# Kernel tuning notes

Measured on AMD Instinct MI355X. Metric: run time of the kernel, lower is better.

Reference implementation:

```python
import jax, jax.numpy as jnp
import numpy as np

N_NODES = 50000
N_EDGES = 800000
D_NODE = 64
D_EDGE = 64


def setup_inputs() -> dict:
    key = jax.random.key(0)
    ks = jax.random.split(key, 6)
    node_scalars = jax.random.normal(ks[0], (N_NODES, D_NODE), dtype=jnp.float32)
    edge_feats = jax.random.normal(ks[1], (N_EDGES, D_EDGE), dtype=jnp.float32)
    src_idxs = jax.random.randint(ks[2], (N_EDGES,), 0, N_NODES, dtype=jnp.int32)
    dst_idxs = jax.random.randint(ks[3], (N_EDGES,), 0, N_NODES, dtype=jnp.int32)
    in_dim = 2 * D_NODE + D_EDGE  # 192
    # He-ish init for the MLP weights
    W1 = jax.random.normal(ks[4], (in_dim, D_EDGE), dtype=jnp.float32) / np.sqrt(in_dim)
    b1 = jnp.zeros((D_EDGE,), dtype=jnp.float32)
    W2 = jax.random.normal(ks[5], (D_EDGE, D_EDGE), dtype=jnp.float32) / np.sqrt(D_EDGE)
    b2 = jnp.zeros((D_EDGE,), dtype=jnp.float32)
    ln_gamma = jnp.ones((D_EDGE,), dtype=jnp.float32)
    ln_beta = jnp.zeros((D_EDGE,), dtype=jnp.float32)
    return {
        "node_scalars": node_scalars,
        "edge_feats": edge_feats,
        "src_idxs": src_idxs,
        "dst_idxs": dst_idxs,
        "W1": W1,
        "b1": b1,
        "W2": W2,
        "b2": b2,
        "ln_gamma": ln_gamma,
        "ln_beta": ln_beta,
    }


def _layer_norm(x, gamma, beta, eps=1e-5):
    mu = jnp.mean(x, axis=-1, keepdims=True)
    var = jnp.mean(jnp.square(x - mu), axis=-1, keepdims=True)
    return (x - mu) * jax.lax.rsqrt(var + eps) * gamma + beta


def reference(node_scalars, edge_feats, src_idxs, dst_idxs, W1, b1, W2, b2, ln_gamma, ln_beta):
    # gather endpoint node features per edge and concat with edge feats -> [E, 2*Dn + De]
    mlp_in = jnp.concatenate(
        [node_scalars[src_idxs], node_scalars[dst_idxs], edge_feats], axis=-1
    )
    h = jax.nn.silu(mlp_in @ W1 + b1)
    h = jax.nn.silu(h @ W2 + b2)
    return _layer_norm(edge_feats + h, ln_gamma, ln_beta)
```

## Files before the change

### kernel.cpp

```cpp
#include <hip/hip_runtime.h>

#define NE 800000
#define D  64
#define K1 192

typedef __bf16 bf16x8 __attribute__((ext_vector_type(8)));
typedef float  f32x4  __attribute__((ext_vector_type(4)));

__global__ void prep_weights(const float* __restrict__ W1,
                             const float* __restrict__ W2,
                             __bf16* __restrict__ ws) {
  int i = blockIdx.x * 256 + threadIdx.x;
  if (i < K1 * D) {
    int k = i >> 6, n = i & 63;
    ws[n * K1 + k] = (__bf16)W1[i];
  } else {
    int j = i - K1 * D;
    int k = j >> 6, n = j & 63;
    ws[K1 * D + n * D + k] = (__bf16)W2[j];
  }
}

template <bool USE_WS>
__global__ __launch_bounds__(256, 3)
void edge_kernel(const float* __restrict__ nodes, const float* __restrict__ ef,
                 const int* __restrict__ srci, const int* __restrict__ dsti,
                 const float* __restrict__ W1, const float* __restrict__ b1,
                 const float* __restrict__ W2, const float* __restrict__ b2,
                 const float* __restrict__ gmm, const float* __restrict__ bta,
                 const __bf16* __restrict__ wsw, float* __restrict__ out) {
  __shared__ __align__(16) __bf16 w1t[64 * 200];
  __shared__ __align__(16) __bf16 w2t[64 * 72];
  __shared__ __align__(16) __bf16 hbuf[4][16 * 72];
  __shared__ float sb1[64], sb2[64], sg[64], sbt[64];

  const int tid = threadIdx.x;

  if (USE_WS) {
    const uint2* s1 = (const uint2*)wsw;
    for (int c = tid; c < 3072; c += 256) {
      int n = c / 48, kc = c - n * 48;
      *(uint2*)&w1t[n * 200 + kc * 4] = s1[c];
    }
    const uint2* s2 = (const uint2*)(wsw + K1 * D);
    for (int c = tid; c < 1024; c += 256) {
      int n = c >> 4, kc = c & 15;
      *(uint2*)&w2t[n * 72 + kc * 4] = s2[c];
    }
  } else {
    for (int i = tid; i < K1 * D; i += 256) {
      int k = i >> 6, n = i & 63;
      w1t[n * 200 + k] = (__bf16)W1[i];
    }
    for (int i = tid; i < D * D; i += 256) {
      int k = i >> 6, n = i & 63;
      w2t[n * 72 + k] = (__bf16)W2[i];
    }
  }
  if (tid < 64)       sb1[tid]       = b1[tid];
  else if (tid < 128) sb2[tid - 64]  = b2[tid - 64];
  else if (tid < 192) sg[tid - 128]  = gmm[tid - 128];
  else                sbt[tid - 192] = bta[tid - 192];
  __syncthreads();

  const int wave = tid >> 6, lane = tid & 63;
  const int quad = lane >> 4, m16 = lane & 15;
  __bf16* hw = hbuf[wave];

  #pragma unroll 1
  for (int t = 0; t < 4; ++t) {
    const int base = blockIdx.x * 256 + wave * 64 + t * 16;
    const int eRow = base + m16;
    const int s = srci[eRow], d = dsti[eRow];
    const float* r0 = nodes + (size_t)s * D;
    const float* r1 = nodes + (size_t)d * D;
    const float* r2 = ef + (size_t)eRow * D;

    f32x4 acc[4] = {};
    #pragma unroll
    for (int ki = 0; ki < 6; ++ki) {
      const float* p;
      if (ki < 2)      p = r0 + ki * 32 + quad * 8;
      else if (ki < 4) p = r1 + (ki - 2) * 32 + quad * 8;
      else             p = r2 + (ki - 4) * 32 + quad * 8;
      f32x4 lo = *(const f32x4*)p;
      f32x4 hi = *(const f32x4*)(p + 4);
      bf16x8 a;
      a[0] = (__bf16)lo[0]; a[1] = (__bf16)lo[1];
      a[2] = (__bf16)lo[2]; a[3] = (__bf16)lo[3];
      a[4] = (__bf16)hi[0]; a[5] = (__bf16)hi[1];
      a[6] = (__bf16)hi[2]; a[7] = (__bf16)hi[3];
      const int wk = ki * 32 + quad * 8;
      #pragma unroll
      for (int nt = 0; nt < 4; ++nt) {
        bf16x8 bf = *(const bf16x8*)&w1t[(nt * 16 + m16) * 200 + wk];
        acc[nt] = __builtin_amdgcn_mfma_f32_16x16x32_bf16(a, bf, acc[nt], 0, 0, 0);
      }
    }

    #pragma unroll
    for (int nt = 0; nt < 4; ++nt) {
      const int c = nt * 16 + m16;
      const float bb = sb1[c];
      #pragma unroll
      for (int r = 0; r < 4; ++r) {
        float x = acc[nt][r] + bb;
        float sv = x / (1.f + __expf(-x));
        hw[(quad * 4 + r) * 72 + c] = (__bf16)sv;
      }
    }
    __syncthreads();

    f32x4 acc2[4] = {};
    #pragma unroll
    for (int ki = 0; ki < 2; ++ki) {
      bf16x8 a = *(const bf16x8*)&hw[m16 * 72 + ki * 32 + quad * 8];
      #pragma unroll
      for (int nt = 0; nt < 4; ++nt) {
        bf16x8 bf = *(const bf16x8*)&w2t[(nt * 16 + m16) * 72 + ki * 32 + quad * 8];
        acc2[nt] = __builtin_amdgcn_mfma_f32_16x16x32_bf16(a, bf, acc2[nt], 0, 0, 0);
      }
    }

    #pragma unroll
    for (int r = 0; r < 4; ++r) {
      const int row = quad * 4 + r;
      const size_t eo = (size_t)(base + row) * D;
      float x[4];
      float sum = 0.f;
      #pragma unroll
      for (int nt = 0; nt < 4; ++nt) {
        const int c = nt * 16 + m16;
        float h = acc2[nt][r] + sb2[c];
        h = h / (1.f + __expf(-h));
        x[nt] = ef[eo + c] + h;
        sum += x[nt];
      }
      float sq = x[0] * x[0] + x[1] * x[1] + x[2] * x[2] + x[3] * x[3];
      #pragma unroll
      for (int off = 1; off < 16; off <<= 1) {
        sum += __shfl_xor(sum, off);
        sq  += __shfl_xor(sq, off);
      }
      const float mean = sum * (1.f / 64.f);
      const float var  = sq * (1.f / 64.f) - mean * mean;
      const float rstd = rsqrtf(var + 1e-5f);
      #pragma unroll
      for (int nt = 0; nt < 4; ++nt) {
        const int c = nt * 16 + m16;
        out[eo + c] = (x[nt] - mean) * rstd * sg[c] + sbt[c];
      }
    }
    __syncthreads();
  }
}

extern "C" void kernel_launch(void* const* d_in, const int* in_sizes, int n_in,
                              void* d_out, int out_size, void* d_ws, size_t ws_size,
                              hipStream_t stream) {
  const float* nodes = (const float*)d_in[0];
  const float* ef    = (const float*)d_in[1];
  const int*   srci  = (const int*)d_in[2];
  const int*   dsti  = (const int*)d_in[3];
  const float* W1    = (const float*)d_in[4];
  const float* b1    = (const float*)d_in[5];
  const float* W2    = (const float*)d_in[6];
  const float* b2    = (const float*)d_in[7];
  const float* gmm   = (const float*)d_in[8];
  const float* bta   = (const float*)d_in[9];
  float* out = (float*)d_out;

  const int blocks = NE / 256;
  if (ws_size >= (size_t)(K1 * D + D * D) * 2) {
    prep_weights<<<64, 256, 0, stream>>>(W1, W2, (__bf16*)d_ws);
    edge_kernel<true><<<blocks, 256, 0, stream>>>(
        nodes, ef, srci, dsti, W1, b1, W2, b2, gmm, bta,
        (const __bf16*)d_ws, out);
  } else {
    edge_kernel<false><<<blocks, 256, 0, stream>>>(
        nodes, ef, srci, dsti, W1, b1, W2, b2, gmm, bta, nullptr, out);
  }
}
```

Measured before the change: 467.6 us.

## Keep W2 fragments in registers and replace block barriers with wave-local LDS fences

Each wave now holds its W2 MFMA B-fragments in registers, loaded once from the bf16 workspace, instead of keeping W2 in LDS. The per-tile __syncthreads calls become s_waitcnt lgkmcnt(0) fences, since each wave only touches its own hbuf slice. SiLU now uses a fast reciprocal instead of a division, and launch bounds target 4 blocks per CU. This removes block-wide barrier stalls and LDS traffic, at the cost of extra registers, and the wave-local fence relies on wave-lockstep ordering between the LDS writes and reads within a wave.

```diff
diff --git a/kernel.cpp b/kernel.cpp
--- a/kernel.cpp
+++ b/kernel.cpp
@@ -21,8 +21,12 @@
   }
 }
 
+__device__ __forceinline__ void wave_lds_fence() {
+  __asm__ volatile("s_waitcnt lgkmcnt(0)" ::: "memory");
+}
+
 template <bool USE_WS>
-__global__ __launch_bounds__(256, 3)
+__global__ __launch_bounds__(256, 4)
 void edge_kernel(const float* __restrict__ nodes, const float* __restrict__ ef,
                  const int* __restrict__ srci, const int* __restrict__ dsti,
                  const float* __restrict__ W1, const float* __restrict__ b1,
@@ -30,11 +34,12 @@
                  const float* __restrict__ gmm, const float* __restrict__ bta,
                  const __bf16* __restrict__ wsw, float* __restrict__ out) {
   __shared__ __align__(16) __bf16 w1t[64 * 200];
-  __shared__ __align__(16) __bf16 w2t[64 * 72];
   __shared__ __align__(16) __bf16 hbuf[4][16 * 72];
   __shared__ float sb1[64], sb2[64], sg[64], sbt[64];
 
   const int tid = threadIdx.x;
+  const int wave = tid >> 6, lane = tid & 63;
+  const int quad = lane >> 4, m16 = lane & 15;
 
   if (USE_WS) {
     const uint2* s1 = (const uint2*)wsw;
@@ -42,29 +47,38 @@
       int n = c / 48, kc = c - n * 48;
       *(uint2*)&w1t[n * 200 + kc * 4] = s1[c];
     }
-    const uint2* s2 = (const uint2*)(wsw + K1 * D);
-    for (int c = tid; c < 1024; c += 256) {
-      int n = c >> 4, kc = c & 15;
-      *(uint2*)&w2t[n * 72 + kc * 4] = s2[c];
-    }
   } else {
     for (int i = tid; i < K1 * D; i += 256) {
       int k = i >> 6, n = i & 63;
       w1t[n * 200 + k] = (__bf16)W1[i];
-    }
-    for (int i = tid; i < D * D; i += 256) {
-      int k = i >> 6, n = i & 63;
-      w2t[n * 72 + k] = (__bf16)W2[i];
     }
   }
   if (tid < 64)       sb1[tid]       = b1[tid];
   else if (tid < 128) sb2[tid - 64]  = b2[tid - 64];
   else if (tid < 192) sg[tid - 128]  = gmm[tid - 128];
   else                sbt[tid - 192] = bta[tid - 192];
+
+  bf16x8 w2f[2][4];
+  if (USE_WS) {
+    const __bf16* w2t = wsw + K1 * D;
+    #pragma unroll
+    for (int ki = 0; ki < 2; ++ki)
+      #pragma unroll
+      for (int nt = 0; nt < 4; ++nt)
+        w2f[ki][nt] = *(const bf16x8*)&w2t[(nt * 16 + m16) * 64 + ki * 32 + quad * 8];
+  } else {
+    #pragma unroll
+    for (int ki = 0; ki < 2; ++ki)
+      #pragma unroll
+      for (int nt = 0; nt < 4; ++nt) {
+        const int n = nt * 16 + m16;
+        #pragma unroll
+        for (int j = 0; j < 8; ++j)
+          w2f[ki][nt][j] = (__bf16)W2[(ki * 32 + quad * 8 + j) * 64 + n];
+      }
+  }
   __syncthreads();
 
-  const int wave = tid >> 6, lane = tid & 63;
-  const int quad = lane >> 4, m16 = lane & 15;
   __bf16* hw = hbuf[wave];
 
   #pragma unroll 1
@@ -105,22 +119,21 @@
       #pragma unroll
       for (int r = 0; r < 4; ++r) {
         float x = acc[nt][r] + bb;
-        float sv = x / (1.f + __expf(-x));
+        float sv = x * __builtin_amdgcn_rcpf(1.f + __expf(-x));
         hw[(quad * 4 + r) * 72 + c] = (__bf16)sv;
       }
     }
-    __syncthreads();
+    wave_lds_fence();
 
     f32x4 acc2[4] = {};
     #pragma unroll
     for (int ki = 0; ki < 2; ++ki) {
       bf16x8 a = *(const bf16x8*)&hw[m16 * 72 + ki * 32 + quad * 8];
       #pragma unroll
-      for (int nt = 0; nt < 4; ++nt) {
-        bf16x8 bf = *(const bf16x8*)&w2t[(nt * 16 + m16) * 72 + ki * 32 + quad * 8];
-        acc2[nt] = __builtin_amdgcn_mfma_f32_16x16x32_bf16(a, bf, acc2[nt], 0, 0, 0);
-      }
+      for (int nt = 0; nt < 4; ++nt)
+        acc2[nt] = __builtin_amdgcn_mfma_f32_16x16x32_bf16(a, w2f[ki][nt], acc2[nt], 0, 0, 0);
     }
+    wave_lds_fence();
 
     #pragma unroll
     for (int r = 0; r < 4; ++r) {
@@ -132,7 +145,7 @@
       for (int nt = 0; nt < 4; ++nt) {
         const int c = nt * 16 + m16;
         float h = acc2[nt][r] + sb2[c];
-        h = h / (1.f + __expf(-h));
+        h = h * __builtin_amdgcn_rcpf(1.f + __expf(-h));
         x[nt] = ef[eo + c] + h;
         sum += x[nt];
       }
@@ -151,7 +164,6 @@
         out[eo + c] = (x[nt] - mean) * rstd * sg[c] + sbt[c];
       }
     }
-    __syncthreads();
   }
 }
 
```

New measurement: 471.0 us. About the same (+0.7%).
